# Optimization experiments

Hardware: AMD Instinct MI355X
Metric: run time of the kernel (lower is better)

Reference implementation:

```python
import jax, jax.numpy as jnp
import numpy as np

NUM_USERS = 100000
NUM_ITEMS = 50000
N = NUM_USERS + NUM_ITEMS
EMBED_DIM = 64
NUM_LAYERS = 3
NNZ = 4800000


def setup_inputs() -> dict:
    key = jax.random.key(0)
    k1, k2, k3, k4, k5 = jax.random.split(key, 5)
    user_emb = jax.random.normal(k1, (NUM_USERS, EMBED_DIM), dtype=jnp.float32)
    item_emb = jax.random.normal(k2, (NUM_ITEMS, EMBED_DIM), dtype=jnp.float32)
    edge_src = jax.random.randint(k3, (NNZ,), 0, N, dtype=jnp.int32)
    edge_dst = jax.random.randint(k4, (NNZ,), 0, N, dtype=jnp.int32)
    edge_val = jax.random.uniform(k5, (NNZ,), dtype=jnp.float32)
    return {"user_emb": user_emb, "item_emb": item_emb,
            "edge_src": edge_src, "edge_dst": edge_dst, "edge_val": edge_val}


def _spmm(edge_src, edge_dst, edge_val, x):
    # y[src] += val * x[dst]   (COO SpMM, fixed sparsity pattern)
    msgs = edge_val[:, None] * x[edge_dst]          # [nnz, D]
    return jax.ops.segment_sum(msgs, edge_src, num_segments=N)


def reference(user_emb, item_emb, edge_src, edge_dst, edge_val):
    ego = jnp.concatenate([user_emb, item_emb], axis=0)  # [N, D]
    acc = ego  # running sum for layer-mean pooling (avoids stacking all layers)
    for _ in range(NUM_LAYERS):
        ego = _spmm(edge_src, edge_dst, edge_val, ego)
        acc = acc + ego
    out = acc / jnp.float32(NUM_LAYERS + 1)  # mean over (num_layers+1) layer embeddings
    user_final = out[:NUM_USERS]
    item_final = out[NUM_USERS:]
    return (user_final, item_final)
```

## Files before the change

### kernel.cpp

```cpp
#include <hip/hip_runtime.h>
#include <hip/hip_fp16.h>

#define NUM_USERS 100000
#define NUM_ITEMS 50000
#define NTOT (NUM_USERS + NUM_ITEMS)
#define EMBED_DIM 64
#define NNZ_E 4800000
#define NUM_LAYERS 3

#define ROWS_PER_BUCKET 256
#define NBUCK ((NTOT + ROWS_PER_BUCKET - 1) / ROWS_PER_BUCKET)
#define BCAP 8960
#define NSUPER 37
#define SCAP 134144
#define EPB1 4096
#define EPB2 4096
#define DMASK 0x3FFFF

__global__ void __launch_bounds__(256)
k_init(const float* __restrict__ ue, const float* __restrict__ ie,
       __half* __restrict__ b0) {
    const long long total2 = (long long)NTOT * EMBED_DIM / 2;
    const long long u2 = (long long)NUM_USERS * EMBED_DIM / 2;
    const float2* ue2 = (const float2*)ue;
    const float2* ie2 = (const float2*)ie;
    __half2* b02 = (__half2*)b0;
    for (long long i = (long long)blockIdx.x * blockDim.x + threadIdx.x;
         i < total2; i += (long long)gridDim.x * blockDim.x) {
        float2 v = (i < u2) ? ue2[i] : ie2[i - u2];
        b02[i] = __floats2half2_rn(v.x, v.y);
    }
}

__global__ void __launch_bounds__(256)
k_super(const int* __restrict__ src, const int* __restrict__ dst,
        const float* __restrict__ val, int* __restrict__ cursorS,
        int2* __restrict__ outS) {
    __shared__ int h[NSUPER];
    __shared__ int base[NSUPER];
    int t = threadIdx.x;
    if (t < NSUPER) h[t] = 0;
    __syncthreads();
    long long e0 = (long long)blockIdx.x * EPB1;
    int n = (int)(((long long)NNZ_E - e0) < EPB1 ? (NNZ_E - e0) : EPB1);
    for (int i = t; i < n; i += 256) {
        int s = __builtin_nontemporal_load(&src[e0 + i]);
        atomicAdd(&h[s >> 12], 1);
    }
    __syncthreads();
    if (t < NSUPER) {
        int c = h[t];
        base[t] = (c > 0) ? atomicAdd(&cursorS[t], c) : 0;
        h[t] = 0;
    }
    __syncthreads();
    for (int i = t; i < n; i += 256) {
        int s = __builtin_nontemporal_load(&src[e0 + i]);
        int d = __builtin_nontemporal_load(&dst[e0 + i]);
        float v = __builtin_nontemporal_load(&val[e0 + i]);
        int sb = s >> 12;
        int off = base[sb] + atomicAdd(&h[sb], 1);
        outS[(long long)sb * SCAP + off] =
            make_int2(d | ((s & 4095) << 18), __float_as_int(v));
    }
}

__global__ void __launch_bounds__(256)
k_bin(const int2* __restrict__ superA, const int* __restrict__ cursorS,
      int* __restrict__ cursorB, int2* __restrict__ outB) {
    __shared__ int h[16];
    __shared__ int base16[16];
    int s = blockIdx.y;
    int cnt = cursorS[s];
    int beg = blockIdx.x * EPB2;
    if (beg >= cnt) return;
    int n = (cnt - beg < EPB2) ? (cnt - beg) : EPB2;
    int t = threadIdx.x;
    const long long* in8 = (const long long*)(superA + (long long)s * SCAP + beg);
    if (t < 16) h[t] = 0;
    __syncthreads();
    for (int i = t; i < n; i += 256) {
        long long raw = __builtin_nontemporal_load(&in8[i]);
        int row12 = ((int)raw >> 18) & 4095;
        atomicAdd(&h[row12 >> 8], 1);
    }
    __syncthreads();
    if (t < 16) {
        int c = h[t];
        base16[t] = (c > 0) ? atomicAdd(&cursorB[s * 16 + t], c) : 0;
        h[t] = 0;
    }
    __syncthreads();
    for (int i = t; i < n; i += 256) {
        long long raw = __builtin_nontemporal_load(&in8[i]);
        int ex = (int)raw;
        int row12 = (ex >> 18) & 4095;
        int bl = row12 >> 8;
        int off = base16[bl] + atomicAdd(&h[bl], 1);
        outB[(long long)(s * 16 + bl) * BCAP + off] =
            make_int2((ex & DMASK) | ((row12 & 255) << 18), (int)(raw >> 32));
    }
}

__global__ void __launch_bounds__(256)
k_sortip(int2* __restrict__ buf, const int* __restrict__ cursor,
         int2* __restrict__ rp) {
    __shared__ int h[ROWS_PER_BUCKET];
    __shared__ int excl[ROWS_PER_BUCKET];
    __shared__ int cur[ROWS_PER_BUCKET];
    __shared__ long long stage[BCAP];
    int b = blockIdx.x;
    int t = threadIdx.x;
    int cnt = cursor[b];
    long long gb = (long long)b * BCAP;
    long long* g8 = (long long*)buf + gb;
    h[t] = 0;
    __syncthreads();
    for (int i = t; i < cnt; i += 256) {
        long long raw = __builtin_nontemporal_load(&g8[i]);
        stage[i] = raw;
        atomicAdd(&h[((int)raw >> 18) & 255], 1);
    }
    __syncthreads();
    int v = h[t];
    excl[t] = v;
    __syncthreads();
    for (int off = 1; off < 256; off <<= 1) {
        int x = (t >= off) ? excl[t - off] : 0;
        __syncthreads();
        excl[t] += x;
        __syncthreads();
    }
    int myExcl = excl[t] - v;
    cur[t] = myExcl;
    int row = b * ROWS_PER_BUCKET + t;
    if (row < NTOT) rp[row] = make_int2((int)(gb + myExcl), (int)(gb + myExcl + v));
    __syncthreads();
    for (int i = t; i < cnt; i += 256) {
        long long raw = stage[i];
        int r = ((int)raw >> 18) & 255;
        int slot = atomicAdd(&cur[r], 1);
        g8[slot] = raw;
    }
}

__device__ __forceinline__ void unpack4(float2 p, float& x0, float& x1,
                                        float& x2, float& x3) {
    __half2 h01 = *(const __half2*)&p.x;
    __half2 h23 = *(const __half2*)&p.y;
    float2 f01 = __half22float2(h01);
    float2 f23 = __half22float2(h23);
    x0 = f01.x; x1 = f01.y; x2 = f23.x; x3 = f23.y;
}

template <int U>
__device__ __forceinline__ void gg(const int2* __restrict__ edges, int j, int grp,
                                   int l16, const float2* __restrict__ xq,
                                   float& a0, float& a1, float& a2, float& a3) {
    int2 e[U];
    float2 xv[U];
#pragma unroll
    for (int k = 0; k < U; ++k) e[k] = edges[j + grp * U + k];
#pragma unroll
    for (int k = 0; k < U; ++k)
        xv[k] = xq[(long long)(e[k].x & DMASK) * 16 + l16];
#pragma unroll
    for (int k = 0; k < U; ++k) {
        float w = __int_as_float(e[k].y);
        float x0, x1, x2, x3;
        unpack4(xv[k], x0, x1, x2, x3);
        a0 = fmaf(w, x0, a0);
        a1 = fmaf(w, x1, a1);
        a2 = fmaf(w, x2, a2);
        a3 = fmaf(w, x3, a3);
    }
}

template <bool LAST>
__global__ void __launch_bounds__(256)
k_spmm_csr(const int2* __restrict__ edges, const int2* __restrict__ rp,
           const __half* __restrict__ x, __half* __restrict__ nxt,
           const __half* __restrict__ eb0, const __half* __restrict__ eb1,
           float* __restrict__ out) {
    int row = blockIdx.x * 4 + (threadIdx.x >> 6);
    int lane = threadIdx.x & 63;
    if (row >= NTOT) return;
    int2 be = rp[row];
    int beg = be.x;
    int end = be.y;
    int grp = lane >> 4;
    int l16 = lane & 15;
    const float2* xq = (const float2*)x;
    float a0 = 0.f, a1 = 0.f, a2 = 0.f, a3 = 0.f;
    int j = beg;
    for (; j + 32 <= end; j += 32) gg<8>(edges, j, grp, l16, xq, a0, a1, a2, a3);
    if (j + 16 <= end) { gg<4>(edges, j, grp, l16, xq, a0, a1, a2, a3); j += 16; }
    if (j + 8 <= end)  { gg<2>(edges, j, grp, l16, xq, a0, a1, a2, a3); j += 8; }
    for (int t2 = j + grp; t2 < end; t2 += 4) {
        int2 e = edges[t2];
        float w = __int_as_float(e.y);
        float x0, x1, x2, x3;
        unpack4(xq[(long long)(e.x & DMASK) * 16 + l16], x0, x1, x2, x3);
        a0 = fmaf(w, x0, a0);
        a1 = fmaf(w, x1, a1);
        a2 = fmaf(w, x2, a2);
        a3 = fmaf(w, x3, a3);
    }
    a0 += __shfl_xor(a0, 16); a1 += __shfl_xor(a1, 16);
    a2 += __shfl_xor(a2, 16); a3 += __shfl_xor(a3, 16);
    a0 += __shfl_xor(a0, 32); a1 += __shfl_xor(a1, 32);
    a2 += __shfl_xor(a2, 32); a3 += __shfl_xor(a3, 32);
    if (grp == 0) {
        if (!LAST) {
            union { __half2 h[2]; float2 f; } u;
            u.h[0] = __floats2half2_rn(a0, a1);
            u.h[1] = __floats2half2_rn(a2, a3);
            ((float2*)nxt)[(long long)row * 16 + l16] = u.f;
        } else {
            float v0, v1, v2, v3, w0, w1, w2, w3, z0, z1, z2, z3;
            unpack4(((const float2*)eb0)[(long long)row * 16 + l16], v0, v1, v2, v3);
            unpack4(((const float2*)eb1)[(long long)row * 16 + l16], w0, w1, w2, w3);
            unpack4(xq[(long long)row * 16 + l16], z0, z1, z2, z3);
            const float s = 1.0f / (NUM_LAYERS + 1);
            float4 r;
            r.x = (v0 + w0 + z0 + a0) * s;
            r.y = (v1 + w1 + z1 + a1) * s;
            r.z = (v2 + w2 + z2 + a2) * s;
            r.w = (v3 + w3 + z3 + a3) * s;
            ((float4*)out)[(long long)row * 16 + l16] = r;
        }
    }
}

extern "C" void kernel_launch(void* const* d_in, const int* in_sizes, int n_in,
                              void* d_out, int out_size, void* d_ws, size_t ws_size,
                              hipStream_t stream) {
    const float* user_emb = (const float*)d_in[0];
    const float* item_emb = (const float*)d_in[1];
    const int* edge_src   = (const int*)d_in[2];
    const int* edge_dst   = (const int*)d_in[3];
    const float* edge_val = (const float*)d_in[4];
    float* out = (float*)d_out;

    auto al = [](size_t x) { return (x + 255) & ~(size_t)255; };
    const size_t halfMat   = (size_t)NTOT * EMBED_DIM * sizeof(__half);
    const size_t buckBytes = al((size_t)NBUCK * BCAP * sizeof(int2));
    const size_t rpBytes   = al(((size_t)NTOT + 8) * sizeof(int2));

    char* p = (char*)d_ws;
    __half* b0 = (__half*)p;
    __half* b1 = (__half*)(p + halfMat);
    __half* b2 = (__half*)(p + 2 * halfMat);
    int2* superA = (int2*)d_ws;
    p += 3 * halfMat;
    int2* bucketedB = (int2*)p;          p += buckBytes;
    int2* rp = (int2*)p;                 p += rpBytes;
    int* cursorS = (int*)p;
    int* cursorB = cursorS + 64;

    hipMemsetAsync(cursorS, 0, 4096, stream);

    hipLaunchKernelGGL(k_super, dim3((NNZ_E + EPB1 - 1) / EPB1), dim3(256), 0,
                       stream, edge_src, edge_dst, edge_val, cursorS, superA);
    hipLaunchKernelGGL(k_bin, dim3((SCAP + EPB2 - 1) / EPB2, NSUPER), dim3(256),
                       0, stream, superA, cursorS, cursorB, bucketedB);
    hipLaunchKernelGGL(k_sortip, dim3(NBUCK), dim3(256), 0, stream,
                       bucketedB, cursorB, rp);
    hipLaunchKernelGGL(k_init, dim3(2048), dim3(256), 0, stream,
                       user_emb, item_emb, b0);

    const int spmmBlocks = (NTOT + 3) / 4;
    hipLaunchKernelGGL((k_spmm_csr<false>), dim3(spmmBlocks), dim3(256), 0,
                       stream, bucketedB, rp, b0, b1,
                       (const __half*)nullptr, (const __half*)nullptr, out);
    hipLaunchKernelGGL((k_spmm_csr<false>), dim3(spmmBlocks), dim3(256), 0,
                       stream, bucketedB, rp, b1, b2,
                       (const __half*)nullptr, (const __half*)nullptr, out);
    hipLaunchKernelGGL((k_spmm_csr<true>), dim3(spmmBlocks), dim3(256), 0,
                       stream, bucketedB, rp, b2, (__half*)nullptr,
                       b0, b1, out);
}
```

Baseline: 418.3 us.

## Halve bucket size to 128 rows, cache src in LDS, widen sort blocks

Cuts the row bucket size from 256 to 128 rows, so there are twice as many buckets, each with a smaller capacity. k_bin now scatters into 32 sub-buckets per super-bucket, and k_sortip runs 512-thread blocks with half-size staging in LDS, which should allow more resident blocks and more parallelism in the in-place counting sort. k_super caches source indices in shared memory so the second pass no longer reloads them from global memory. The risk is tighter per-bucket capacity (overflow if the degree distribution is skewed) and half the threads sitting idle during the 128-entry scan.

```diff
diff --git a/kernel.cpp b/kernel.cpp
--- a/kernel.cpp
+++ b/kernel.cpp
@@ -8,9 +8,9 @@
 #define NNZ_E 4800000
 #define NUM_LAYERS 3
 
-#define ROWS_PER_BUCKET 256
-#define NBUCK ((NTOT + ROWS_PER_BUCKET - 1) / ROWS_PER_BUCKET)
-#define BCAP 8960
+#define RPB 128
+#define NBUCK ((NTOT + RPB - 1) / RPB)
+#define BCAP 4672
 #define NSUPER 37
 #define SCAP 134144
 #define EPB1 4096
@@ -38,6 +38,7 @@
         int2* __restrict__ outS) {
     __shared__ int h[NSUPER];
     __shared__ int base[NSUPER];
+    __shared__ int srcbuf[EPB1];
     int t = threadIdx.x;
     if (t < NSUPER) h[t] = 0;
     __syncthreads();
@@ -45,6 +46,7 @@
     int n = (int)(((long long)NNZ_E - e0) < EPB1 ? (NNZ_E - e0) : EPB1);
     for (int i = t; i < n; i += 256) {
         int s = __builtin_nontemporal_load(&src[e0 + i]);
+        srcbuf[i] = s;
         atomicAdd(&h[s >> 12], 1);
     }
     __syncthreads();
@@ -55,7 +57,7 @@
     }
     __syncthreads();
     for (int i = t; i < n; i += 256) {
-        int s = __builtin_nontemporal_load(&src[e0 + i]);
+        int s = srcbuf[i];
         int d = __builtin_nontemporal_load(&dst[e0 + i]);
         float v = __builtin_nontemporal_load(&val[e0 + i]);
         int sb = s >> 12;
@@ -68,8 +70,8 @@
 __global__ void __launch_bounds__(256)
 k_bin(const int2* __restrict__ superA, const int* __restrict__ cursorS,
       int* __restrict__ cursorB, int2* __restrict__ outB) {
-    __shared__ int h[16];
-    __shared__ int base16[16];
+    __shared__ int h[32];
+    __shared__ int base32[32];
     int s = blockIdx.y;
     int cnt = cursorS[s];
     int beg = blockIdx.x * EPB2;
@@ -77,17 +79,17 @@
     int n = (cnt - beg < EPB2) ? (cnt - beg) : EPB2;
     int t = threadIdx.x;
     const long long* in8 = (const long long*)(superA + (long long)s * SCAP + beg);
-    if (t < 16) h[t] = 0;
+    if (t < 32) h[t] = 0;
     __syncthreads();
     for (int i = t; i < n; i += 256) {
         long long raw = __builtin_nontemporal_load(&in8[i]);
         int row12 = ((int)raw >> 18) & 4095;
-        atomicAdd(&h[row12 >> 8], 1);
-    }
-    __syncthreads();
-    if (t < 16) {
+        atomicAdd(&h[row12 >> 7], 1);
+    }
+    __syncthreads();
+    if (t < 32) {
         int c = h[t];
-        base16[t] = (c > 0) ? atomicAdd(&cursorB[s * 16 + t], c) : 0;
+        base32[t] = (c > 0) ? atomicAdd(&cursorB[s * 32 + t], c) : 0;
         h[t] = 0;
     }
     __syncthreads();
@@ -95,50 +97,54 @@
         long long raw = __builtin_nontemporal_load(&in8[i]);
         int ex = (int)raw;
         int row12 = (ex >> 18) & 4095;
-        int bl = row12 >> 8;
-        int off = base16[bl] + atomicAdd(&h[bl], 1);
-        outB[(long long)(s * 16 + bl) * BCAP + off] =
-            make_int2((ex & DMASK) | ((row12 & 255) << 18), (int)(raw >> 32));
-    }
-}
-
-__global__ void __launch_bounds__(256)
+        int bl = row12 >> 7;
+        int off = base32[bl] + atomicAdd(&h[bl], 1);
+        outB[(long long)(s * 32 + bl) * BCAP + off] =
+            make_int2((ex & DMASK) | ((row12 & 127) << 18), (int)(raw >> 32));
+    }
+}
+
+__global__ void __launch_bounds__(512)
 k_sortip(int2* __restrict__ buf, const int* __restrict__ cursor,
          int2* __restrict__ rp) {
-    __shared__ int h[ROWS_PER_BUCKET];
-    __shared__ int excl[ROWS_PER_BUCKET];
-    __shared__ int cur[ROWS_PER_BUCKET];
+    __shared__ int h[RPB];
+    __shared__ int excl[RPB];
+    __shared__ int cur[RPB];
     __shared__ long long stage[BCAP];
     int b = blockIdx.x;
     int t = threadIdx.x;
     int cnt = cursor[b];
     long long gb = (long long)b * BCAP;
     long long* g8 = (long long*)buf + gb;
-    h[t] = 0;
-    __syncthreads();
-    for (int i = t; i < cnt; i += 256) {
+    if (t < RPB) h[t] = 0;
+    __syncthreads();
+    for (int i = t; i < cnt; i += 512) {
         long long raw = __builtin_nontemporal_load(&g8[i]);
         stage[i] = raw;
-        atomicAdd(&h[((int)raw >> 18) & 255], 1);
-    }
-    __syncthreads();
-    int v = h[t];
-    excl[t] = v;
-    __syncthreads();
-    for (int off = 1; off < 256; off <<= 1) {
-        int x = (t >= off) ? excl[t - off] : 0;
+        atomicAdd(&h[((int)raw >> 18) & 127], 1);
+    }
+    __syncthreads();
+    int v = 0;
+    if (t < RPB) { v = h[t]; excl[t] = v; }
+    __syncthreads();
+    for (int off = 1; off < RPB; off <<= 1) {
+        int x = 0;
+        if (t < RPB && t >= off) x = excl[t - off];
         __syncthreads();
-        excl[t] += x;
+        if (t < RPB) excl[t] += x;
         __syncthreads();
     }
-    int myExcl = excl[t] - v;
-    cur[t] = myExcl;
-    int row = b * ROWS_PER_BUCKET + t;
-    if (row < NTOT) rp[row] = make_int2((int)(gb + myExcl), (int)(gb + myExcl + v));
-    __syncthreads();
-    for (int i = t; i < cnt; i += 256) {
+    if (t < RPB) {
+        int myExcl = excl[t] - v;
+        cur[t] = myExcl;
+        int row = b * RPB + t;
+        if (row < NTOT)
+            rp[row] = make_int2((int)(gb + myExcl), (int)(gb + myExcl + v));
+    }
+    __syncthreads();
+    for (int i = t; i < cnt; i += 512) {
         long long raw = stage[i];
-        int r = ((int)raw >> 18) & 255;
+        int r = ((int)raw >> 18) & 127;
         int slot = atomicAdd(&cur[r], 1);
         g8[slot] = raw;
     }
@@ -258,13 +264,13 @@
     int* cursorS = (int*)p;
     int* cursorB = cursorS + 64;
 
-    hipMemsetAsync(cursorS, 0, 4096, stream);
+    hipMemsetAsync(cursorS, 0, 8192, stream);
 
     hipLaunchKernelGGL(k_super, dim3((NNZ_E + EPB1 - 1) / EPB1), dim3(256), 0,
                        stream, edge_src, edge_dst, edge_val, cursorS, superA);
     hipLaunchKernelGGL(k_bin, dim3((SCAP + EPB2 - 1) / EPB2, NSUPER), dim3(256),
                        0, stream, superA, cursorS, cursorB, bucketedB);
-    hipLaunchKernelGGL(k_sortip, dim3(NBUCK), dim3(256), 0, stream,
+    hipLaunchKernelGGL(k_sortip, dim3(NBUCK), dim3(512), 0, stream,
                        bucketedB, cursorB, rp);
     hipLaunchKernelGGL(k_init, dim3(2048), dim3(256), 0, stream,
                        user_emb, item_emb, b0);
```

New measurement: 409.9 us, median of 2. 1.02x faster.
